# Performance work log

Measured on AMD Instinct MI355X. Metric: run time of the kernel, lower is better.

## Reference

```python
import jax, jax.numpy as jnp
import numpy as np
from math import sqrt

KEY_DIM = 128
VALUE_DIM = 128
SUMMARY_DIM = 128
QUESTION_NUM = 10000
CONCEPT_NUM = 64
B = 128
S = 128


def setup_inputs() -> dict:
    key = jax.random.key(0)
    ks = jax.random.split(key, 24)
    stdev = 1.0 / sqrt(CONCEPT_NUM + KEY_DIM)

    def lin_w(k, out_f, in_f):
        bound = 1.0 / sqrt(in_f)
        return jax.random.uniform(k, (out_f, in_f), jnp.float32, -bound, bound)

    def lin_b(k, out_f, in_f):
        bound = 1.0 / sqrt(in_f)
        return jax.random.uniform(k, (out_f,), jnp.float32, -bound, bound)

    q_emb = jax.random.normal(ks[0], (QUESTION_NUM + 1, KEY_DIM), jnp.float32)
    q_emb = q_emb.at[0].set(0.0)  # padding_idx = 0
    i_emb = jax.random.normal(ks[1], (2 * QUESTION_NUM + 1, VALUE_DIM), jnp.float32)
    i_emb = i_emb.at[0].set(0.0)

    inp = {
        "right_input": jax.random.randint(ks[2], (B, S), 0, 2 * QUESTION_NUM + 1),
        "wrong_input": jax.random.randint(ks[3], (B, S), 0, 2 * QUESTION_NUM + 1),
        "target_id": jax.random.randint(ks[4], (B,), 0, QUESTION_NUM + 1),
        "q_emb": q_emb,
        "i_emb": i_emb,
        "key_W": lin_w(ks[5], CONCEPT_NUM, KEY_DIM),  # no bias
        "erase_W": lin_w(ks[6], VALUE_DIM, VALUE_DIM),
        "erase_b": lin_b(ks[7], VALUE_DIM, VALUE_DIM),
        "add_W": lin_w(ks[8], VALUE_DIM, VALUE_DIM),
        "add_b": lin_b(ks[9], VALUE_DIM, VALUE_DIM),
        "rsum_W": lin_w(ks[10], SUMMARY_DIM, VALUE_DIM + KEY_DIM),
        "rsum_b": lin_b(ks[11], SUMMARY_DIM, VALUE_DIM + KEY_DIM),
        "wsum_W": lin_w(ks[12], SUMMARY_DIM, VALUE_DIM + KEY_DIM),
        "wsum_b": lin_b(ks[13], SUMMARY_DIM, VALUE_DIM + KEY_DIM),
        "succ_W": lin_w(ks[14], 1, SUMMARY_DIM),
        "succ_b": lin_b(ks[15], 1, SUMMARY_DIM),
        "fail_W": lin_w(ks[16], 1, SUMMARY_DIM),
        "fail_b": lin_b(ks[17], 1, SUMMARY_DIM),
        "diff_W": lin_w(ks[18], 1, KEY_DIM),
        "diff_b": lin_b(ks[19], 1, KEY_DIM),
        "right_mem_init": jax.random.uniform(ks[20], (VALUE_DIM, CONCEPT_NUM), jnp.float32, -stdev, stdev),
        "wrong_mem_init": jax.random.uniform(ks[21], (VALUE_DIM, CONCEPT_NUM), jnp.float32, -stdev, stdev),
    }
    return inp


def reference(right_input, wrong_input, target_id, q_emb, i_emb, key_W,
              erase_W, erase_b, add_W, add_b, rsum_W, rsum_b, wsum_W, wsum_b,
              succ_W, succ_b, fail_W, fail_b, diff_W, diff_b,
              right_mem_init, wrong_mem_init):
    Q = (i_emb.shape[0] - 1) // 2
    batch = right_input.shape[0]

    def corr(qid):  # (B,) -> (B, C) correlation weights
        return jax.nn.softmax(q_emb[qid] @ key_W.T, axis=-1)

    def update(mem, inter):
        # mem: (B, V, C); inter: (B,) interaction ids
        vec = i_emb[inter]                                  # (B, V)
        e = jax.nn.sigmoid(vec @ erase_W.T + erase_b)       # (B, V)
        a = jnp.tanh(vec @ add_W.T + add_b)                 # (B, V)
        qid = inter - Q * (inter > Q).astype(inter.dtype)
        w = corr(qid)                                       # (B, C)
        # erase/add are outer products w (x) e, w (x) a -> (B, V, C)
        return mem * (1.0 - e[:, :, None] * w[:, None, :]) + a[:, :, None] * w[:, None, :]

    def step(carry, xs):
        rm, wm = carry
        ri, wi = xs
        return (update(rm, ri), update(wm, wi)), None

    rm0 = jnp.broadcast_to(right_mem_init, (batch,) + right_mem_init.shape)
    wm0 = jnp.broadcast_to(wrong_mem_init, (batch,) + wrong_mem_init.shape)
    (rm, wm), _ = jax.lax.scan(step, (rm0, wm0), (right_input.T, wrong_input.T))

    qv = q_emb[target_id]                                   # (B, K)
    w_t = corr(target_id)                                   # (B, C)
    right_read = jnp.einsum('bvc,bc->bv', rm, w_t)          # (B, V)
    wrong_read = jnp.einsum('bvc,bc->bv', wm, w_t)

    r_sum = jnp.tanh(jnp.concatenate([right_read, qv], axis=-1) @ rsum_W.T + rsum_b)
    w_sum = jnp.tanh(jnp.concatenate([wrong_read, qv], axis=-1) @ wsum_W.T + wsum_b)

    success_level = jnp.tanh(r_sum @ succ_W.T + succ_b)     # (B, 1)
    failure_level = jnp.tanh(w_sum @ fail_W.T + fail_b)     # (B, 1)
    difficulty_level = jnp.tanh(qv @ diff_W.T + diff_b)     # (B, 1)

    success_count = jnp.sum(jnp.clip(right_input, 0, 1)).astype(jnp.float32)
    failure_count = jnp.sum(jnp.clip(wrong_input, 0, 1)).astype(jnp.float32)

    out = (success_level * jax.nn.sigmoid(success_count)
           + failure_level * jax.nn.sigmoid(failure_count)
           - difficulty_level * 2.0)
    return out
```

## Files before the change

### kernel.cpp

```cpp
#include <hip/hip_runtime.h>
#include <hip/hip_bf16.h>

#define BB 128
#define SS 128
#define VD 128
#define CN 64
#define KD 128
#define QN 10000
#define MROWS (2*BB*SS)
#define MTOT  (MROWS + BB)

typedef __attribute__((ext_vector_type(8))) short bf16x8;
typedef __attribute__((ext_vector_type(4))) float f32x4;

__device__ __forceinline__ float bflo(unsigned int u) { return __uint_as_float(u << 16); }
__device__ __forceinline__ float bfhi(unsigned int u) { return __uint_as_float(u & 0xffff0000u); }
__device__ __forceinline__ unsigned short f2bf(float f) {
    unsigned int x = __float_as_uint(f);
    return (unsigned short)((x + 0x7fffu + ((x >> 16) & 1u)) >> 16);
}
__device__ __forceinline__ unsigned int pk2(float lo, float hi) {
    return (unsigned int)f2bf(lo) | ((unsigned int)f2bf(hi) << 16);
}
__device__ __forceinline__ float fast_tanh(float x) {
    float e = __expf(2.0f * x);
    return 1.0f - 2.0f / (e + 1.0f);
}
__device__ __forceinline__ float fast_sig(float x) {
    return 1.0f / (1.0f + __expf(-x));
}

__global__ __launch_bounds__(256) void k_wcnt(
    const float* __restrict__ erase_W, const float* __restrict__ add_W,
    const float* __restrict__ key_W, unsigned short* __restrict__ Bfrag,
    const int* __restrict__ ri, const int* __restrict__ wi, float* __restrict__ sig)
{
    if (blockIdx.x < 20) {
        const int bid = blockIdx.x * 4 + (threadIdx.x >> 6);
        const int l = threadIdx.x & 63;
        const int n = (bid >> 2) * 16 + (l & 15);
        const int k0 = (bid & 3) * 32 + (l >> 4) * 8;
        const float* src;
        if (n < 128)      src = erase_W + (size_t)n * KD + k0;
        else if (n < 256) src = add_W + (size_t)(n - 128) * KD + k0;
        else              src = key_W + (size_t)(n - 256) * KD + k0;
        float4 fa = ((const float4*)src)[0];
        float4 fb = ((const float4*)src)[1];
        uint4 o = make_uint4(pk2(fa.x, fa.y), pk2(fa.z, fa.w), pk2(fb.x, fb.y), pk2(fb.z, fb.w));
        *(uint4*)(Bfrag + ((size_t)bid * 64 + l) * 8) = o;
    } else {
        __shared__ int sr_s[4], sw_s[4];
        const int t = threadIdx.x;
        const int4* r4 = (const int4*)ri;
        const int4* w4 = (const int4*)wi;
        int sr = 0, sw = 0;
        #pragma unroll 4
        for (int p = 0; p < 16; ++p) {
            int4 a = r4[p * 256 + t];
            int4 b = w4[p * 256 + t];
            sr += (a.x >= 1) + (a.y >= 1) + (a.z >= 1) + (a.w >= 1);
            sw += (b.x >= 1) + (b.y >= 1) + (b.z >= 1) + (b.w >= 1);
        }
        for (int off = 1; off < 64; off <<= 1) { sr += __shfl_xor(sr, off); sw += __shfl_xor(sw, off); }
        int wid = t >> 6;
        if ((t & 63) == 0) { sr_s[wid] = sr; sw_s[wid] = sw; }
        __syncthreads();
        if (t == 0) {
            int SR = sr_s[0]+sr_s[1]+sr_s[2]+sr_s[3];
            int SW = sw_s[0]+sw_s[1]+sw_s[2]+sw_s[3];
            sig[0] = 1.0f / (1.0f + __expf(-(float)SR));
            sig[1] = 1.0f / (1.0f + __expf(-(float)SW));
        }
    }
}

__global__ __launch_bounds__(256) void k_mfma(
    const int* __restrict__ ri, const int* __restrict__ wi, const int* __restrict__ tgt,
    const float* __restrict__ q_emb, const float* __restrict__ i_emb,
    const float* __restrict__ erase_b, const float* __restrict__ add_b,
    const unsigned short* __restrict__ Bfrag,
    unsigned int* __restrict__ EAbuf,
    unsigned short* __restrict__ Wbf, float* __restrict__ WTbuf)
{
    __shared__ __align__(16) char shA[32 * 256];
    __shared__ __align__(16) char shB[32 * 68 * 4];
    __shared__ int id_s[32], ir_s[32];

    const int t = threadIdx.x;
    const int lane = t & 63;
    const int w = t >> 6;
    const int base = blockIdx.x * 32;
    const bool ea = (base < MROWS);

    if (t < 32) {
        int r = base + t;
        int irow = 0, qid;
        if (r < MROWS) {
            int m = r >> 14;
            int idx = r & 16383;
            int inter = (m == 0) ? ri[idx] : wi[idx];
            irow = inter;
            qid = (inter > QN) ? inter - QN : inter;
        } else {
            qid = tgt[r - MROWS];
        }
        id_s[t] = qid; ir_s[t] = irow;
    }
    __syncthreads();

    {
        const int r = t >> 3, o = t & 7;
        const int bb = r * 256 + o * 32;
        const int sw = (r & 7) << 4;
        {
            const float* src = q_emb + (size_t)id_s[r] * KD + o * 16;
            float4 f0 = ((const float4*)src)[0];
            float4 f1 = ((const float4*)src)[1];
            float4 f2 = ((const float4*)src)[2];
            float4 f3 = ((const float4*)src)[3];
            *(uint4*)(shB + (bb ^ sw))        = make_uint4(pk2(f0.x,f0.y), pk2(f0.z,f0.w), pk2(f1.x,f1.y), pk2(f1.z,f1.w));
            *(uint4*)(shB + ((bb + 16) ^ sw)) = make_uint4(pk2(f2.x,f2.y), pk2(f2.z,f2.w), pk2(f3.x,f3.y), pk2(f3.z,f3.w));
        }
        if (ea) {
            const float* src = i_emb + (size_t)ir_s[r] * KD + o * 16;
            float4 f0 = ((const float4*)src)[0];
            float4 f1 = ((const float4*)src)[1];
            float4 f2 = ((const float4*)src)[2];
            float4 f3 = ((const float4*)src)[3];
            *(uint4*)(shA + (bb ^ sw))        = make_uint4(pk2(f0.x,f0.y), pk2(f0.z,f0.w), pk2(f1.x,f1.y), pk2(f1.z,f1.w));
            *(uint4*)(shA + ((bb + 16) ^ sw)) = make_uint4(pk2(f2.x,f2.y), pk2(f2.z,f2.w), pk2(f3.x,f3.y), pk2(f3.z,f3.w));
        }
    }
    __syncthreads();

    const int rowl = lane & 15;
    const int kb16 = (lane >> 4) * 16;

    bf16x8 afQ[2][4];
    #pragma unroll
    for (int mt = 0; mt < 2; ++mt)
        #pragma unroll
        for (int kt = 0; kt < 4; ++kt) {
            int row = mt * 16 + rowl;
            int addr = (row * 256 + kt * 64 + kb16) ^ ((row & 7) << 4);
            afQ[mt][kt] = *(const bf16x8*)(shB + addr);
        }

    f32x4 accK0 = {0.f,0.f,0.f,0.f}, accK1 = {0.f,0.f,0.f,0.f};
    {
        const int gk = 16 + w;
        #pragma unroll
        for (int kt = 0; kt < 4; ++kt) {
            bf16x8 bf = *(const bf16x8*)(Bfrag + ((size_t)(gk * 4 + kt) * 64 + lane) * 8);
            accK0 = __builtin_amdgcn_mfma_f32_16x16x32_bf16(afQ[0][kt], bf, accK0, 0, 0, 0);
            accK1 = __builtin_amdgcn_mfma_f32_16x16x32_bf16(afQ[1][kt], bf, accK1, 0, 0, 0);
        }
    }
    __syncthreads();

    {
        float* L = (float*)shB;
        const int col = w * 16 + rowl;
        const int rb4 = (lane >> 4) * 4;
        #pragma unroll
        for (int rr = 0; rr < 4; ++rr) L[(rb4 + rr) * 68 + col] = accK0[rr];
        #pragma unroll
        for (int rr = 0; rr < 4; ++rr) L[(16 + rb4 + rr) * 68 + col] = accK1[rr];
    }
    __syncthreads();

    {
        const float* L = (const float*)shB;
        const int rr = t >> 3, q = t & 7;
        float4 va = *(const float4*)(L + rr * 68 + q * 8);
        float4 vb = *(const float4*)(L + rr * 68 + q * 8 + 4);
        float mx = fmaxf(fmaxf(fmaxf(va.x, va.y), fmaxf(va.z, va.w)),
                         fmaxf(fmaxf(vb.x, vb.y), fmaxf(vb.z, vb.w)));
        #pragma unroll
        for (int off = 1; off < 8; off <<= 1) mx = fmaxf(mx, __shfl_xor(mx, off));
        float e0 = __expf(va.x - mx), e1 = __expf(va.y - mx), e2 = __expf(va.z - mx), e3 = __expf(va.w - mx);
        float e4 = __expf(vb.x - mx), e5 = __expf(vb.y - mx), e6 = __expf(vb.z - mx), e7 = __expf(vb.w - mx);
        float s = e0 + e1 + e2 + e3 + e4 + e5 + e6 + e7;
        #pragma unroll
        for (int off = 1; off < 8; off <<= 1) s += __shfl_xor(s, off);
        float inv = 1.0f / s;
        int R = base + rr;
        if (R < MROWS) {
            uint4 o = make_uint4(pk2(e0*inv, e1*inv), pk2(e2*inv, e3*inv),
                                 pk2(e4*inv, e5*inv), pk2(e6*inv, e7*inv));
            *(uint4*)(Wbf + (size_t)R * CN + q * 8) = o;
        } else {
            float* dst = WTbuf + (size_t)(R - MROWS) * CN + q * 8;
            *(float4*)dst       = make_float4(e0*inv, e1*inv, e2*inv, e3*inv);
            *(float4*)(dst + 4) = make_float4(e4*inv, e5*inv, e6*inv, e7*inv);
        }
    }

    if (ea) {
        bf16x8 afI[2][4];
        #pragma unroll
        for (int mt = 0; mt < 2; ++mt)
            #pragma unroll
            for (int kt = 0; kt < 4; ++kt) {
                int row = mt * 16 + rowl;
                int addr = (row * 256 + kt * 64 + kb16) ^ ((row & 7) << 4);
                afI[mt][kt] = *(const bf16x8*)(shA + addr);
            }

        const int rb4 = (lane >> 4) * 4;
        f32x4 accE[2][2], accA[2][2];
        #pragma unroll
        for (int gi = 0; gi < 4; ++gi) {
            const int g = w + gi * 4;
            f32x4 a0 = {0.f,0.f,0.f,0.f}, a1 = {0.f,0.f,0.f,0.f};
            #pragma unroll
            for (int kt = 0; kt < 4; ++kt) {
                bf16x8 bf = *(const bf16x8*)(Bfrag + ((size_t)(g * 4 + kt) * 64 + lane) * 8);
                a0 = __builtin_amdgcn_mfma_f32_16x16x32_bf16(afI[0][kt], bf, a0, 0, 0, 0);
                a1 = __builtin_amdgcn_mfma_f32_16x16x32_bf16(afI[1][kt], bf, a1, 0, 0, 0);
            }
            if (gi < 2) { accE[gi][0] = a0; accE[gi][1] = a1; }
            else        { accA[gi - 2][0] = a0; accA[gi - 2][1] = a1; }
        }
        #pragma unroll
        for (int ci = 0; ci < 2; ++ci) {
            const int cc = ci * 64 + w * 16 + rowl;
            const float bvE = erase_b[cc];
            const float bvA = add_b[cc];
            #pragma unroll
            for (int mt = 0; mt < 2; ++mt) {
                #pragma unroll
                for (int rr = 0; rr < 4; ++rr) {
                    float e = fast_sig(accE[ci][mt][rr] + bvE);
                    float a = fast_tanh(accA[ci][mt][rr] + bvA);
                    EAbuf[(size_t)(base + mt * 16 + rb4 + rr) * VD + cc] = pk2(e, a);
                }
            }
        }
    }
}

__global__ __launch_bounds__(512, 2) void k_scan(
    const unsigned int* __restrict__ EAbuf, const unsigned short* __restrict__ Wbf,
    const float* __restrict__ WTbuf,
    const float* __restrict__ rmem0, const float* __restrict__ wmem0,
    float* __restrict__ readbuf)
{
    __shared__ unsigned int lds_ea[SS * VD];
    __shared__ unsigned short lds_w[SS * CN];
    __shared__ float psum[8 * 64];
    const int t = threadIdx.x;
    const int chain = blockIdx.x;
    const int m = chain >> 7;
    const int b = chain & 127;
    const int lane = t & 63;
    const int w = t >> 6;
    const int vhalf = w & 1;
    const int cq = w >> 1;
    const int vg = lane >> 2;
    const int cg = lane & 3;
    const int v0 = vhalf * 64 + vg * 4;
    const int c0 = cq * 16 + cg * 4;

    {
        const uint4* sEA = (const uint4*)(EAbuf + (size_t)chain * SS * VD);
        uint4* dEA = (uint4*)lds_ea;
        #pragma unroll
        for (int i = 0; i < 8; ++i) dEA[t + i * 512] = sEA[t + i * 512];
        const uint4* sW = (const uint4*)(Wbf + (size_t)chain * SS * CN);
        uint4* dW = (uint4*)lds_w;
        dW[t] = sW[t];
        dW[t + 512] = sW[t + 512];
    }

    const float* minit = (m == 0) ? rmem0 : wmem0;
    float mm[4][4];
    #pragma unroll
    for (int j = 0; j < 4; ++j) {
        float4 mi = *(const float4*)(minit + (v0 + j) * CN + c0);
        mm[j][0] = mi.x; mm[j][1] = mi.y; mm[j][2] = mi.z; mm[j][3] = mi.w;
    }
    __syncthreads();

    for (int so = 0; so < 32; ++so) {
        #pragma unroll
        for (int kk = 0; kk < 4; ++kk) {
            const int s = so * 4 + kk;
            uint4 ea = *(const uint4*)(lds_ea + s * VD + v0);
            uint2 wu = *(const uint2*)(lds_w + s * CN + c0);
            float e[4] = { bflo(ea.x), bflo(ea.y), bflo(ea.z), bflo(ea.w) };
            float a[4] = { bfhi(ea.x), bfhi(ea.y), bfhi(ea.z), bfhi(ea.w) };
            float wv[4] = { bflo(wu.x), bfhi(wu.x), bflo(wu.y), bfhi(wu.y) };
            #pragma unroll
            for (int j = 0; j < 4; ++j) {
                #pragma unroll
                for (int k = 0; k < 4; ++k) {
                    float g = fmaf(-e[j], mm[j][k], a[j]);
                    mm[j][k] = fmaf(wv[k], g, mm[j][k]);
                }
            }
        }
    }

    float4 wt = *(const float4*)(WTbuf + (size_t)b * CN + c0);
    float p[4];
    #pragma unroll
    for (int j = 0; j < 4; ++j) {
        float x = mm[j][0] * wt.x;
        x = fmaf(mm[j][1], wt.y, x);
        x = fmaf(mm[j][2], wt.z, x);
        x = fmaf(mm[j][3], wt.w, x);
        p[j] = x;
    }
    #pragma unroll
    for (int j = 0; j < 4; ++j) {
        p[j] += __shfl_xor(p[j], 1);
        p[j] += __shfl_xor(p[j], 2);
    }
    if (cg == 0) {
        #pragma unroll
        for (int j = 0; j < 4; ++j) psum[w * 64 + vg * 4 + j] = p[j];
    }
    __syncthreads();
    if (t < 128) {
        const int vh = t >> 6, vl = t & 63;
        float s = psum[(0 * 2 + vh) * 64 + vl] + psum[(1 * 2 + vh) * 64 + vl]
                + psum[(2 * 2 + vh) * 64 + vl] + psum[(3 * 2 + vh) * 64 + vl];
        readbuf[(size_t)chain * VD + t] = s;
    }
}

__global__ __launch_bounds__(256) void k_head(
    const float* __restrict__ readbuf, const int* __restrict__ tgt,
    const float* __restrict__ q_emb,
    const float* __restrict__ rsum_W, const float* __restrict__ rsum_b,
    const float* __restrict__ wsum_W, const float* __restrict__ wsum_b,
    const float* __restrict__ succ_W, const float* __restrict__ succ_b,
    const float* __restrict__ fail_W, const float* __restrict__ fail_b,
    const float* __restrict__ diff_W, const float* __restrict__ diff_b,
    const float* __restrict__ sig, float* __restrict__ out)
{
    __shared__ float xr[256], xw[256];
    __shared__ float part[2][128];
    __shared__ float red_s[6];
    const int t = threadIdx.x;
    const int j = t & 127;
    const int h = t >> 7;
    const int b = blockIdx.x;
    if (h == 0) {
        int tid_ = tgt[b];
        float qv = q_emb[(size_t)tid_ * KD + j];
        xr[j]       = readbuf[(size_t)b * VD + j];
        xr[128 + j] = qv;
        xw[j]       = readbuf[(size_t)(BB + b) * VD + j];
        xw[128 + j] = qv;
    }
    __syncthreads();

    float rs = (h == 0) ? rsum_b[j] : 0.0f;
    float wv = (h == 0) ? wsum_b[j] : 0.0f;
    const float* rw = rsum_W + (size_t)j * 256 + h * 128;
    const float* ww = wsum_W + (size_t)j * 256 + h * 128;
    const float* xrp = xr + h * 128;
    const float* xwp = xw + h * 128;
    #pragma unroll 4
    for (int k = 0; k < 128; ++k) {
        rs = fmaf(rw[k], xrp[k], rs);
        wv = fmaf(ww[k], xwp[k], wv);
    }
    if (h == 1) { part[0][j] = rs; part[1][j] = wv; }
    __syncthreads();
    if (h == 0) {
        rs += part[0][j];
        wv += part[1][j];
        float r_sum = fast_tanh(rs), w_sum = fast_tanh(wv);
        float qv = xr[128 + j];
        float ps = r_sum * succ_W[j];
        float pf = w_sum * fail_W[j];
        float pd = qv    * diff_W[j];
        for (int off = 1; off < 64; off <<= 1) {
            ps += __shfl_xor(ps, off);
            pf += __shfl_xor(pf, off);
            pd += __shfl_xor(pd, off);
        }
        int wid = j >> 6;
        if ((j & 63) == 0) { red_s[wid*3+0] = ps; red_s[wid*3+1] = pf; red_s[wid*3+2] = pd; }
    }
    __syncthreads();
    if (t == 0) {
        float Ps = red_s[0] + red_s[3];
        float Pf = red_s[1] + red_s[4];
        float Pd = red_s[2] + red_s[5];
        float succ = fast_tanh(Ps + succ_b[0]);
        float fail = fast_tanh(Pf + fail_b[0]);
        float diff = fast_tanh(Pd + diff_b[0]);
        out[b] = succ * sig[0] + fail * sig[1] - 2.0f * diff;
    }
}

extern "C" void kernel_launch(void* const* d_in, const int* in_sizes, int n_in,
                              void* d_out, int out_size, void* d_ws, size_t ws_size,
                              hipStream_t stream) {
    const int*   ri      = (const int*)d_in[0];
    const int*   wi      = (const int*)d_in[1];
    const int*   tgt     = (const int*)d_in[2];
    const float* q_emb   = (const float*)d_in[3];
    const float* i_emb   = (const float*)d_in[4];
    const float* key_W   = (const float*)d_in[5];
    const float* erase_W = (const float*)d_in[6];
    const float* erase_b = (const float*)d_in[7];
    const float* add_W   = (const float*)d_in[8];
    const float* add_b   = (const float*)d_in[9];
    const float* rsum_W  = (const float*)d_in[10];
    const float* rsum_b  = (const float*)d_in[11];
    const float* wsum_W  = (const float*)d_in[12];
    const float* wsum_b  = (const float*)d_in[13];
    const float* succ_W  = (const float*)d_in[14];
    const float* succ_b  = (const float*)d_in[15];
    const float* fail_W  = (const float*)d_in[16];
    const float* fail_b  = (const float*)d_in[17];
    const float* diff_W  = (const float*)d_in[18];
    const float* diff_b  = (const float*)d_in[19];
    const float* rmem0   = (const float*)d_in[20];
    const float* wmem0   = (const float*)d_in[21];

    char* ws = (char*)d_ws;
    unsigned int*   EAbuf   = (unsigned int*)(ws + 0);
    unsigned short* Wbf     = (unsigned short*)(ws + 16777216);
    float*          WTbuf   = (float*)(ws + 20971520);
    float*          readbuf = (float*)(ws + 21004288);
    unsigned short* Bfrag   = (unsigned short*)(ws + 21135360);
    float*          sig     = (float*)(ws + 21217280);
    float*          out     = (float*)d_out;

    hipLaunchKernelGGL(k_wcnt, dim3(21), dim3(256), 0, stream,
        erase_W, add_W, key_W, Bfrag, ri, wi, sig);
    hipLaunchKernelGGL(k_mfma, dim3(1028), dim3(256), 0, stream,
        ri, wi, tgt, q_emb, i_emb, erase_b, add_b, Bfrag,
        EAbuf, Wbf, WTbuf);
    hipLaunchKernelGGL(k_scan, dim3(256), dim3(512), 0, stream,
        EAbuf, Wbf, WTbuf, rmem0, wmem0, readbuf);
    hipLaunchKernelGGL(k_head, dim3(128), dim3(256), 0, stream,
        readbuf, tgt, q_emb, rsum_W, rsum_b, wsum_W, wsum_b,
        succ_W, succ_b, fail_W, fail_b, diff_W, diff_b, sig, out);
}
```

Before: 57.86 us.

## Fuse embedding MFMA and softmax stage into per-chain scan kernel

The separate MFMA kernel that wrote erase/add gates and attention weights to global workspace is merged into the scan kernel. Each chain block now gathers its 128 question and interaction embeddings, runs the key and erase/add MFMAs, applies the softmax, and writes the results straight into LDS. The target-weight softmax is recomputed per block from key_W in fp32. This removes the roughly 20 MB global write and read-back plus one kernel launch. In exchange the pre-scan work runs on only 256 blocks with very high LDS use (about 148 KB per block), and the scan loop unroll goes from 4 to 8.

```diff
diff --git a/kernel.cpp b/kernel.cpp
--- a/kernel.cpp
+++ b/kernel.cpp
@@ -7,8 +7,6 @@
 #define CN 64
 #define KD 128
 #define QN 10000
-#define MROWS (2*BB*SS)
-#define MTOT  (MROWS + BB)
 
 typedef __attribute__((ext_vector_type(8))) short bf16x8;
 typedef __attribute__((ext_vector_type(4))) float f32x4;
@@ -74,205 +72,191 @@
     }
 }
 
-__global__ __launch_bounds__(256) void k_mfma(
+__global__ __launch_bounds__(512, 2) void k_chain(
     const int* __restrict__ ri, const int* __restrict__ wi, const int* __restrict__ tgt,
     const float* __restrict__ q_emb, const float* __restrict__ i_emb,
+    const float* __restrict__ key_W,
     const float* __restrict__ erase_b, const float* __restrict__ add_b,
     const unsigned short* __restrict__ Bfrag,
-    unsigned int* __restrict__ EAbuf,
-    unsigned short* __restrict__ Wbf, float* __restrict__ WTbuf)
+    const float* __restrict__ rmem0, const float* __restrict__ wmem0,
+    float* __restrict__ readbuf)
 {
-    __shared__ __align__(16) char shA[32 * 256];
-    __shared__ __align__(16) char shB[32 * 68 * 4];
-    __shared__ int id_s[32], ir_s[32];
+    __shared__ __align__(16) unsigned int lds_ea[SS * VD];
+    __shared__ __align__(16) char xab[32 * 1024];
+    __shared__ __align__(16) float logits[SS * 68];
+    __shared__ __align__(16) unsigned short lds_w[SS * CN];
+    __shared__ float q_t[KD];
+    __shared__ float logit_t[CN];
+    __shared__ float wt_lds[CN];
+    __shared__ int qid_s[SS], ir_s[SS];
+    __shared__ float psum[8 * 64];
 
     const int t = threadIdx.x;
     const int lane = t & 63;
     const int w = t >> 6;
-    const int base = blockIdx.x * 32;
-    const bool ea = (base < MROWS);
-
-    if (t < 32) {
-        int r = base + t;
-        int irow = 0, qid;
-        if (r < MROWS) {
-            int m = r >> 14;
-            int idx = r & 16383;
-            int inter = (m == 0) ? ri[idx] : wi[idx];
-            irow = inter;
-            qid = (inter > QN) ? inter - QN : inter;
-        } else {
-            qid = tgt[r - MROWS];
-        }
-        id_s[t] = qid; ir_s[t] = irow;
+    const int chain = blockIdx.x;
+    const int m = chain >> 7;
+    const int b = chain & 127;
+
+    if (t < SS) {
+        int inter = (m == 0 ? ri : wi)[b * SS + t];
+        ir_s[t] = inter;
+        qid_s[t] = (inter > QN) ? inter - QN : inter;
+        q_t[t] = q_emb[(size_t)tgt[b] * KD + t];
     }
     __syncthreads();
 
     {
-        const int r = t >> 3, o = t & 7;
-        const int bb = r * 256 + o * 32;
-        const int sw = (r & 7) << 4;
-        {
-            const float* src = q_emb + (size_t)id_s[r] * KD + o * 16;
+        const int r0 = t >> 3, o = t & 7;
+        #pragma unroll
+        for (int h = 0; h < 2; ++h) {
+            const int r = r0 + h * 64;
+            const float* src = q_emb + (size_t)qid_s[r] * KD + o * 16;
             float4 f0 = ((const float4*)src)[0];
             float4 f1 = ((const float4*)src)[1];
             float4 f2 = ((const float4*)src)[2];
             float4 f3 = ((const float4*)src)[3];
-            *(uint4*)(shB + (bb ^ sw))        = make_uint4(pk2(f0.x,f0.y), pk2(f0.z,f0.w), pk2(f1.x,f1.y), pk2(f1.z,f1.w));
-            *(uint4*)(shB + ((bb + 16) ^ sw)) = make_uint4(pk2(f2.x,f2.y), pk2(f2.z,f2.w), pk2(f3.x,f3.y), pk2(f3.z,f3.w));
-        }
-        if (ea) {
+            const int bb = r * 256 + o * 32;
+            const int sw = (r & 7) << 4;
+            *(uint4*)(xab + (bb ^ sw))        = make_uint4(pk2(f0.x,f0.y), pk2(f0.z,f0.w), pk2(f1.x,f1.y), pk2(f1.z,f1.w));
+            *(uint4*)(xab + ((bb + 16) ^ sw)) = make_uint4(pk2(f2.x,f2.y), pk2(f2.z,f2.w), pk2(f3.x,f3.y), pk2(f3.z,f3.w));
+        }
+        const int c = t >> 3, oct = t & 7;
+        const float* kw = key_W + (size_t)c * KD + oct * 16;
+        float s = 0.f;
+        #pragma unroll
+        for (int i = 0; i < 16; ++i) s = fmaf(kw[i], q_t[oct * 16 + i], s);
+        s += __shfl_xor(s, 1); s += __shfl_xor(s, 2); s += __shfl_xor(s, 4);
+        if (oct == 0) logit_t[c] = s;
+    }
+    __syncthreads();
+
+    const int rowl = lane & 15;
+    const int kb16 = (lane >> 4) * 16;
+    const int rb4 = (lane >> 4) * 4;
+
+    {
+        if (w == 0) {
+            float x = logit_t[lane];
+            float mx = x;
+            #pragma unroll
+            for (int off = 1; off < 64; off <<= 1) mx = fmaxf(mx, __shfl_xor(mx, off));
+            float e = __expf(x - mx);
+            float ssum = e;
+            #pragma unroll
+            for (int off = 1; off < 64; off <<= 1) ssum += __shfl_xor(ssum, off);
+            wt_lds[lane] = e / ssum;
+        }
+        bf16x8 afQ[4];
+        const int row = w * 16 + rowl;
+        #pragma unroll
+        for (int kt = 0; kt < 4; ++kt)
+            afQ[kt] = *(const bf16x8*)(xab + ((row * 256 + kt * 64 + kb16) ^ ((row & 7) << 4)));
+        #pragma unroll
+        for (int nt = 0; nt < 4; ++nt) {
+            f32x4 acc = {0.f,0.f,0.f,0.f};
+            #pragma unroll
+            for (int kt = 0; kt < 4; ++kt) {
+                bf16x8 bf = *(const bf16x8*)(Bfrag + ((size_t)((16 + nt) * 4 + kt) * 64 + lane) * 8);
+                acc = __builtin_amdgcn_mfma_f32_16x16x32_bf16(afQ[kt], bf, acc, 0, 0, 0);
+            }
+            #pragma unroll
+            for (int rr = 0; rr < 4; ++rr)
+                logits[(w * 16 + rb4 + rr) * 68 + nt * 16 + rowl] = acc[rr];
+        }
+    }
+    __syncthreads();
+
+    {
+        const int r0 = t >> 3, o = t & 7;
+        uint4 xi[2][2];
+        #pragma unroll
+        for (int h = 0; h < 2; ++h) {
+            const int r = r0 + h * 64;
             const float* src = i_emb + (size_t)ir_s[r] * KD + o * 16;
             float4 f0 = ((const float4*)src)[0];
             float4 f1 = ((const float4*)src)[1];
             float4 f2 = ((const float4*)src)[2];
             float4 f3 = ((const float4*)src)[3];
-            *(uint4*)(shA + (bb ^ sw))        = make_uint4(pk2(f0.x,f0.y), pk2(f0.z,f0.w), pk2(f1.x,f1.y), pk2(f1.z,f1.w));
-            *(uint4*)(shA + ((bb + 16) ^ sw)) = make_uint4(pk2(f2.x,f2.y), pk2(f2.z,f2.w), pk2(f3.x,f3.y), pk2(f3.z,f3.w));
-        }
-    }
-    __syncthreads();
-
-    const int rowl = lane & 15;
-    const int kb16 = (lane >> 4) * 16;
-
-    bf16x8 afQ[2][4];
-    #pragma unroll
-    for (int mt = 0; mt < 2; ++mt)
-        #pragma unroll
-        for (int kt = 0; kt < 4; ++kt) {
-            int row = mt * 16 + rowl;
-            int addr = (row * 256 + kt * 64 + kb16) ^ ((row & 7) << 4);
-            afQ[mt][kt] = *(const bf16x8*)(shB + addr);
-        }
-
-    f32x4 accK0 = {0.f,0.f,0.f,0.f}, accK1 = {0.f,0.f,0.f,0.f};
-    {
-        const int gk = 16 + w;
-        #pragma unroll
-        for (int kt = 0; kt < 4; ++kt) {
-            bf16x8 bf = *(const bf16x8*)(Bfrag + ((size_t)(gk * 4 + kt) * 64 + lane) * 8);
-            accK0 = __builtin_amdgcn_mfma_f32_16x16x32_bf16(afQ[0][kt], bf, accK0, 0, 0, 0);
-            accK1 = __builtin_amdgcn_mfma_f32_16x16x32_bf16(afQ[1][kt], bf, accK1, 0, 0, 0);
-        }
-    }
-    __syncthreads();
-
-    {
-        float* L = (float*)shB;
-        const int col = w * 16 + rowl;
-        const int rb4 = (lane >> 4) * 4;
-        #pragma unroll
-        for (int rr = 0; rr < 4; ++rr) L[(rb4 + rr) * 68 + col] = accK0[rr];
-        #pragma unroll
-        for (int rr = 0; rr < 4; ++rr) L[(16 + rb4 + rr) * 68 + col] = accK1[rr];
-    }
-    __syncthreads();
-
-    {
-        const float* L = (const float*)shB;
-        const int rr = t >> 3, q = t & 7;
-        float4 va = *(const float4*)(L + rr * 68 + q * 8);
-        float4 vb = *(const float4*)(L + rr * 68 + q * 8 + 4);
+            xi[h][0] = make_uint4(pk2(f0.x,f0.y), pk2(f0.z,f0.w), pk2(f1.x,f1.y), pk2(f1.z,f1.w));
+            xi[h][1] = make_uint4(pk2(f2.x,f2.y), pk2(f2.z,f2.w), pk2(f3.x,f3.y), pk2(f3.z,f3.w));
+        }
+
+        const int rr = t >> 2, q4 = t & 3;
+        const float* L = logits + rr * 68 + q4 * 16;
+        float4 va = ((const float4*)L)[0];
+        float4 vb = ((const float4*)L)[1];
+        float4 vc = ((const float4*)L)[2];
+        float4 vd = ((const float4*)L)[3];
         float mx = fmaxf(fmaxf(fmaxf(va.x, va.y), fmaxf(va.z, va.w)),
                          fmaxf(fmaxf(vb.x, vb.y), fmaxf(vb.z, vb.w)));
-        #pragma unroll
-        for (int off = 1; off < 8; off <<= 1) mx = fmaxf(mx, __shfl_xor(mx, off));
-        float e0 = __expf(va.x - mx), e1 = __expf(va.y - mx), e2 = __expf(va.z - mx), e3 = __expf(va.w - mx);
-        float e4 = __expf(vb.x - mx), e5 = __expf(vb.y - mx), e6 = __expf(vb.z - mx), e7 = __expf(vb.w - mx);
-        float s = e0 + e1 + e2 + e3 + e4 + e5 + e6 + e7;
-        #pragma unroll
-        for (int off = 1; off < 8; off <<= 1) s += __shfl_xor(s, off);
+        mx = fmaxf(mx, fmaxf(fmaxf(fmaxf(vc.x, vc.y), fmaxf(vc.z, vc.w)),
+                             fmaxf(fmaxf(vd.x, vd.y), fmaxf(vd.z, vd.w))));
+        mx = fmaxf(mx, __shfl_xor(mx, 1));
+        mx = fmaxf(mx, __shfl_xor(mx, 2));
+        float ex[16];
+        ex[0] = __expf(va.x - mx); ex[1] = __expf(va.y - mx); ex[2] = __expf(va.z - mx); ex[3] = __expf(va.w - mx);
+        ex[4] = __expf(vb.x - mx); ex[5] = __expf(vb.y - mx); ex[6] = __expf(vb.z - mx); ex[7] = __expf(vb.w - mx);
+        ex[8] = __expf(vc.x - mx); ex[9] = __expf(vc.y - mx); ex[10] = __expf(vc.z - mx); ex[11] = __expf(vc.w - mx);
+        ex[12] = __expf(vd.x - mx); ex[13] = __expf(vd.y - mx); ex[14] = __expf(vd.z - mx); ex[15] = __expf(vd.w - mx);
+        float s = 0.f;
+        #pragma unroll
+        for (int i = 0; i < 16; ++i) s += ex[i];
+        s += __shfl_xor(s, 1);
+        s += __shfl_xor(s, 2);
         float inv = 1.0f / s;
-        int R = base + rr;
-        if (R < MROWS) {
-            uint4 o = make_uint4(pk2(e0*inv, e1*inv), pk2(e2*inv, e3*inv),
-                                 pk2(e4*inv, e5*inv), pk2(e6*inv, e7*inv));
-            *(uint4*)(Wbf + (size_t)R * CN + q * 8) = o;
-        } else {
-            float* dst = WTbuf + (size_t)(R - MROWS) * CN + q * 8;
-            *(float4*)dst       = make_float4(e0*inv, e1*inv, e2*inv, e3*inv);
-            *(float4*)(dst + 4) = make_float4(e4*inv, e5*inv, e6*inv, e7*inv);
-        }
-    }
-
-    if (ea) {
-        bf16x8 afI[2][4];
-        #pragma unroll
-        for (int mt = 0; mt < 2; ++mt)
+        uint4 o0 = make_uint4(pk2(ex[0]*inv, ex[1]*inv), pk2(ex[2]*inv, ex[3]*inv),
+                              pk2(ex[4]*inv, ex[5]*inv), pk2(ex[6]*inv, ex[7]*inv));
+        uint4 o1 = make_uint4(pk2(ex[8]*inv, ex[9]*inv), pk2(ex[10]*inv, ex[11]*inv),
+                              pk2(ex[12]*inv, ex[13]*inv), pk2(ex[14]*inv, ex[15]*inv));
+        *(uint4*)(lds_w + rr * CN + q4 * 16)     = o0;
+        *(uint4*)(lds_w + rr * CN + q4 * 16 + 8) = o1;
+
+        #pragma unroll
+        for (int h = 0; h < 2; ++h) {
+            const int r = r0 + h * 64;
+            const int bb = r * 256 + o * 32;
+            const int sw = (r & 7) << 4;
+            *(uint4*)(xab + (bb ^ sw))        = xi[h][0];
+            *(uint4*)(xab + ((bb + 16) ^ sw)) = xi[h][1];
+        }
+    }
+    __syncthreads();
+
+    {
+        bf16x8 afI[4];
+        const int row = w * 16 + rowl;
+        #pragma unroll
+        for (int kt = 0; kt < 4; ++kt)
+            afI[kt] = *(const bf16x8*)(xab + ((row * 256 + kt * 64 + kb16) ^ ((row & 7) << 4)));
+        #pragma unroll
+        for (int ci = 0; ci < 8; ++ci) {
+            f32x4 ae = {0.f,0.f,0.f,0.f}, aa = {0.f,0.f,0.f,0.f};
             #pragma unroll
             for (int kt = 0; kt < 4; ++kt) {
-                int row = mt * 16 + rowl;
-                int addr = (row * 256 + kt * 64 + kb16) ^ ((row & 7) << 4);
-                afI[mt][kt] = *(const bf16x8*)(shA + addr);
+                bf16x8 be = *(const bf16x8*)(Bfrag + ((size_t)(ci * 4 + kt) * 64 + lane) * 8);
+                bf16x8 ba = *(const bf16x8*)(Bfrag + ((size_t)((8 + ci) * 4 + kt) * 64 + lane) * 8);
+                ae = __builtin_amdgcn_mfma_f32_16x16x32_bf16(afI[kt], be, ae, 0, 0, 0);
+                aa = __builtin_amdgcn_mfma_f32_16x16x32_bf16(afI[kt], ba, aa, 0, 0, 0);
             }
-
-        const int rb4 = (lane >> 4) * 4;
-        f32x4 accE[2][2], accA[2][2];
-        #pragma unroll
-        for (int gi = 0; gi < 4; ++gi) {
-            const int g = w + gi * 4;
-            f32x4 a0 = {0.f,0.f,0.f,0.f}, a1 = {0.f,0.f,0.f,0.f};
-            #pragma unroll
-            for (int kt = 0; kt < 4; ++kt) {
-                bf16x8 bf = *(const bf16x8*)(Bfrag + ((size_t)(g * 4 + kt) * 64 + lane) * 8);
-                a0 = __builtin_amdgcn_mfma_f32_16x16x32_bf16(afI[0][kt], bf, a0, 0, 0, 0);
-                a1 = __builtin_amdgcn_mfma_f32_16x16x32_bf16(afI[1][kt], bf, a1, 0, 0, 0);
-            }
-            if (gi < 2) { accE[gi][0] = a0; accE[gi][1] = a1; }
-            else        { accA[gi - 2][0] = a0; accA[gi - 2][1] = a1; }
-        }
-        #pragma unroll
-        for (int ci = 0; ci < 2; ++ci) {
-            const int cc = ci * 64 + w * 16 + rowl;
+            const int cc = ci * 16 + rowl;
             const float bvE = erase_b[cc];
             const float bvA = add_b[cc];
             #pragma unroll
-            for (int mt = 0; mt < 2; ++mt) {
-                #pragma unroll
-                for (int rr = 0; rr < 4; ++rr) {
-                    float e = fast_sig(accE[ci][mt][rr] + bvE);
-                    float a = fast_tanh(accA[ci][mt][rr] + bvA);
-                    EAbuf[(size_t)(base + mt * 16 + rb4 + rr) * VD + cc] = pk2(e, a);
-                }
+            for (int rr = 0; rr < 4; ++rr) {
+                float e = fast_sig(ae[rr] + bvE);
+                float a = fast_tanh(aa[rr] + bvA);
+                lds_ea[(w * 16 + rb4 + rr) * VD + cc] = pk2(e, a);
             }
         }
     }
-}
-
-__global__ __launch_bounds__(512, 2) void k_scan(
-    const unsigned int* __restrict__ EAbuf, const unsigned short* __restrict__ Wbf,
-    const float* __restrict__ WTbuf,
-    const float* __restrict__ rmem0, const float* __restrict__ wmem0,
-    float* __restrict__ readbuf)
-{
-    __shared__ unsigned int lds_ea[SS * VD];
-    __shared__ unsigned short lds_w[SS * CN];
-    __shared__ float psum[8 * 64];
-    const int t = threadIdx.x;
-    const int chain = blockIdx.x;
-    const int m = chain >> 7;
-    const int b = chain & 127;
-    const int lane = t & 63;
-    const int w = t >> 6;
+
     const int vhalf = w & 1;
     const int cq = w >> 1;
     const int vg = lane >> 2;
     const int cg = lane & 3;
     const int v0 = vhalf * 64 + vg * 4;
     const int c0 = cq * 16 + cg * 4;
-
-    {
-        const uint4* sEA = (const uint4*)(EAbuf + (size_t)chain * SS * VD);
-        uint4* dEA = (uint4*)lds_ea;
-        #pragma unroll
-        for (int i = 0; i < 8; ++i) dEA[t + i * 512] = sEA[t + i * 512];
-        const uint4* sW = (const uint4*)(Wbf + (size_t)chain * SS * CN);
-        uint4* dW = (uint4*)lds_w;
-        dW[t] = sW[t];
-        dW[t + 512] = sW[t + 512];
-    }
-
     const float* minit = (m == 0) ? rmem0 : wmem0;
     float mm[4][4];
     #pragma unroll
@@ -282,10 +266,10 @@
     }
     __syncthreads();
 
-    for (int so = 0; so < 32; ++so) {
-        #pragma unroll
-        for (int kk = 0; kk < 4; ++kk) {
-            const int s = so * 4 + kk;
+    for (int so = 0; so < 16; ++so) {
+        #pragma unroll
+        for (int kk = 0; kk < 8; ++kk) {
+            const int s = so * 8 + kk;
             uint4 ea = *(const uint4*)(lds_ea + s * VD + v0);
             uint2 wu = *(const uint2*)(lds_w + s * CN + c0);
             float e[4] = { bflo(ea.x), bflo(ea.y), bflo(ea.z), bflo(ea.w) };
@@ -302,7 +286,7 @@
         }
     }
 
-    float4 wt = *(const float4*)(WTbuf + (size_t)b * CN + c0);
+    float4 wt = *(const float4*)(wt_lds + c0);
     float p[4];
     #pragma unroll
     for (int j = 0; j < 4; ++j) {
@@ -425,21 +409,16 @@
     const float* wmem0   = (const float*)d_in[21];
 
     char* ws = (char*)d_ws;
-    unsigned int*   EAbuf   = (unsigned int*)(ws + 0);
-    unsigned short* Wbf     = (unsigned short*)(ws + 16777216);
-    float*          WTbuf   = (float*)(ws + 20971520);
-    float*          readbuf = (float*)(ws + 21004288);
-    unsigned short* Bfrag   = (unsigned short*)(ws + 21135360);
-    float*          sig     = (float*)(ws + 21217280);
+    float*          readbuf = (float*)(ws + 0);
+    unsigned short* Bfrag   = (unsigned short*)(ws + 131072);
+    float*          sig     = (float*)(ws + 212992);
     float*          out     = (float*)d_out;
 
     hipLaunchKernelGGL(k_wcnt, dim3(21), dim3(256), 0, stream,
         erase_W, add_W, key_W, Bfrag, ri, wi, sig);
-    hipLaunchKernelGGL(k_mfma, dim3(1028), dim3(256), 0, stream,
-        ri, wi, tgt, q_emb, i_emb, erase_b, add_b, Bfrag,
-        EAbuf, Wbf, WTbuf);
-    hipLaunchKernelGGL(k_scan, dim3(256), dim3(512), 0, stream,
-        EAbuf, Wbf, WTbuf, rmem0, wmem0, readbuf);
+    hipLaunchKernelGGL(k_chain, dim3(256), dim3(512), 0, stream,
+        ri, wi, tgt, q_emb, i_emb, key_W, erase_b, add_b, Bfrag,
+        rmem0, wmem0, readbuf);
     hipLaunchKernelGGL(k_head, dim3(128), dim3(256), 0, stream,
         readbuf, tgt, q_emb, rsum_W, rsum_b, wsum_W, wsum_b,
         succ_W, succ_b, fail_W, fail_b, diff_W, diff_b, sig, out);
```

Result: faster. 50.58 us (-12.6%).
